# Kernel tuning notes

Hardware: AMD Instinct MI355X
Metric: run time of the kernel (lower is better)

## Reference

```python
import jax, jax.numpy as jnp
import numpy as np

N = 33_554_432  # 2**25 elements, 128 MB fp32

def setup_inputs() -> dict:
    key = jax.random.key(0)
    x = jax.random.normal(key, (N,), dtype=jnp.float32)
    return {"x": x}

def reference(x):
    # Faithful semantics of the original module (dim=0, 1-D input):
    # iteration i writes the scalar prefix sum P_{i+1}=sum(x[:i+1]) into
    # positions 0..i (broadcasting copy_). Every position j is last written
    # at iteration i = n-1, so the final tensor is sum(x) everywhere.
    total = jnp.sum(x)
    return jnp.full_like(x, total)
```

## Files before the change

### kernel.cpp

```cpp
#include <hip/hip_runtime.h>


#define NBLK 2048
#define NTHR 256

typedef float vfloat4 __attribute__((ext_vector_type(4)));

__global__ __launch_bounds__(NTHR) void reduce_partial_kernel(
    const vfloat4* __restrict__ x4, const float* __restrict__ x,
    float* __restrict__ partials, int n4, int n)
{
    int tid    = blockIdx.x * blockDim.x + threadIdx.x;
    int stride = gridDim.x * blockDim.x;

    float s = 0.0f;
    for (int i = tid; i < n4; i += stride) {
        vfloat4 v = x4[i];
        s += (v.x + v.y) + (v.z + v.w);
    }
    int tail_start = n4 * 4;
    int tail_n = n - tail_start;
    if (tid < tail_n) s += x[tail_start + tid];

    #pragma unroll
    for (int off = 32; off > 0; off >>= 1)
        s += __shfl_down(s, off, 64);

    __shared__ float smem[NTHR / 64];
    int lane = threadIdx.x & 63;
    int wid  = threadIdx.x >> 6;
    if (lane == 0) smem[wid] = s;
    __syncthreads();
    if (threadIdx.x == 0) {
        float t = 0.0f;
        #pragma unroll
        for (int w = 0; w < NTHR / 64; ++w) t += smem[w];
        partials[blockIdx.x] = t;
    }
}

__global__ __launch_bounds__(NTHR) void fill_total_kernel(
    vfloat4* __restrict__ out4, float* __restrict__ out,
    const float* __restrict__ partials, int n4, int n)
{
    float s = 0.0f;
    for (int i = threadIdx.x; i < NBLK; i += NTHR) s += partials[i];

    #pragma unroll
    for (int off = 32; off > 0; off >>= 1)
        s += __shfl_down(s, off, 64);

    __shared__ float smem[NTHR / 64];
    __shared__ float total_sh;
    int lane = threadIdx.x & 63;
    int wid  = threadIdx.x >> 6;
    if (lane == 0) smem[wid] = s;
    __syncthreads();
    if (threadIdx.x == 0) {
        float t = 0.0f;
        #pragma unroll
        for (int w = 0; w < NTHR / 64; ++w) t += smem[w];
        total_sh = t;
    }
    __syncthreads();

    float t = total_sh;
    vfloat4 v = { t, t, t, t };

    int tid    = blockIdx.x * blockDim.x + threadIdx.x;
    int stride = gridDim.x * blockDim.x;
    for (int i = tid; i < n4; i += stride)
        __builtin_nontemporal_store(v, &out4[i]);

    int tail_start = n4 * 4;
    int tail_n = n - tail_start;
    if (tid < tail_n) out[tail_start + tid] = t;
}

extern "C" void kernel_launch(void* const* d_in, const int* in_sizes, int n_in,
                              void* d_out, int out_size, void* d_ws, size_t ws_size,
                              hipStream_t stream)
{
    const float*   x    = (const float*)d_in[0];
    const vfloat4* x4   = (const vfloat4*)d_in[0];
    float*         out  = (float*)d_out;
    vfloat4*       out4 = (vfloat4*)d_out;

    int n  = in_sizes[0];
    int n4 = n / 4;

    float* partials = (float*)d_ws;

    reduce_partial_kernel<<<NBLK, NTHR, 0, stream>>>(x4, x, partials, n4, n);
    fill_total_kernel<<<NBLK, NTHR, 0, stream>>>(out4, out, partials, n4, out_size);
}
```

Before: 56.98 us.

## Fuse reduction and fill into one cooperative kernel with grid sync

Merges the partial-sum kernel and the fill kernel into a single cooperative launch, using a grid-wide sync between the reduction and the broadcast fill. This removes the second kernel launch and its gap. The partials are now read with float4 loads, and the fill switches from nontemporal to ordinary stores. It requires all 2048 blocks to be co-resident and adds grid-barrier cost. The fill passes n where the old code passed out_size, which only matters if the two differ.

```diff
diff --git a/kernel.cpp b/kernel.cpp
--- a/kernel.cpp
+++ b/kernel.cpp
@@ -1,4 +1,7 @@
 #include <hip/hip_runtime.h>
+#include <hip/hip_cooperative_groups.h>
+
+namespace cg = cooperative_groups;
 
 
 #define NBLK 2048
@@ -6,12 +9,21 @@
 
 typedef float vfloat4 __attribute__((ext_vector_type(4)));
 
-__global__ __launch_bounds__(NTHR) void reduce_partial_kernel(
+__global__ __launch_bounds__(NTHR, 8) void fused_sum_fill_kernel(
     const vfloat4* __restrict__ x4, const float* __restrict__ x,
-    float* __restrict__ partials, int n4, int n)
+    float* __restrict__ partials,
+    vfloat4* __restrict__ out4, float* __restrict__ out,
+    int n4, int n)
 {
+    cg::grid_group grid = cg::this_grid();
+
+    __shared__ float smem[NTHR / 64];
+    __shared__ float total_sh;
+
     int tid    = blockIdx.x * blockDim.x + threadIdx.x;
     int stride = gridDim.x * blockDim.x;
+    int lane   = threadIdx.x & 63;
+    int wid    = threadIdx.x >> 6;
 
     float s = 0.0f;
     for (int i = tid; i < n4; i += stride) {
@@ -26,9 +38,6 @@
     for (int off = 32; off > 0; off >>= 1)
         s += __shfl_down(s, off, 64);
 
-    __shared__ float smem[NTHR / 64];
-    int lane = threadIdx.x & 63;
-    int wid  = threadIdx.x >> 6;
     if (lane == 0) smem[wid] = s;
     __syncthreads();
     if (threadIdx.x == 0) {
@@ -37,24 +46,21 @@
         for (int w = 0; w < NTHR / 64; ++w) t += smem[w];
         partials[blockIdx.x] = t;
     }
-}
 
-__global__ __launch_bounds__(NTHR) void fill_total_kernel(
-    vfloat4* __restrict__ out4, float* __restrict__ out,
-    const float* __restrict__ partials, int n4, int n)
-{
-    float s = 0.0f;
-    for (int i = threadIdx.x; i < NBLK; i += NTHR) s += partials[i];
+    grid.sync();
 
+    const vfloat4* p4 = (const vfloat4*)partials;
+    float r = 0.0f;
+    #pragma unroll
+    for (int k = 0; k < NBLK / 4 / NTHR; ++k) {
+        vfloat4 v = p4[threadIdx.x + k * NTHR];
+        r += (v.x + v.y) + (v.z + v.w);
+    }
     #pragma unroll
     for (int off = 32; off > 0; off >>= 1)
-        s += __shfl_down(s, off, 64);
+        r += __shfl_down(r, off, 64);
 
-    __shared__ float smem[NTHR / 64];
-    __shared__ float total_sh;
-    int lane = threadIdx.x & 63;
-    int wid  = threadIdx.x >> 6;
-    if (lane == 0) smem[wid] = s;
+    if (lane == 0) smem[wid] = r;
     __syncthreads();
     if (threadIdx.x == 0) {
         float t = 0.0f;
@@ -67,13 +73,8 @@
     float t = total_sh;
     vfloat4 v = { t, t, t, t };
 
-    int tid    = blockIdx.x * blockDim.x + threadIdx.x;
-    int stride = gridDim.x * blockDim.x;
     for (int i = tid; i < n4; i += stride)
-        __builtin_nontemporal_store(v, &out4[i]);
-
-    int tail_start = n4 * 4;
-    int tail_n = n - tail_start;
+        out4[i] = v;
     if (tid < tail_n) out[tail_start + tid] = t;
 }
 
@@ -91,6 +92,8 @@
 
     float* partials = (float*)d_ws;
 
-    reduce_partial_kernel<<<NBLK, NTHR, 0, stream>>>(x4, x, partials, n4, n);
-    fill_total_kernel<<<NBLK, NTHR, 0, stream>>>(out4, out, partials, n4, out_size);
+    void* args[] = { (void*)&x4, (void*)&x, (void*)&partials,
+                     (void*)&out4, (void*)&out, (void*)&n4, (void*)&n };
+    hipLaunchCooperativeKernel((const void*)fused_sum_fill_kernel,
+                               dim3(NBLK), dim3(NTHR), args, 0, stream);
 }
```

Result: slower. 154.9 us (+171.9%).
